# Optimization experiments

Measured on AMD Instinct MI355X. Metric: run time of the kernel, lower is better.

Reference implementation:

```python
import jax, jax.numpy as jnp
import numpy as np

LAMBDA_COORD = 5.0
LAMBDA_NOOBJ = 0.5


def _iou(box1, box2):
    # boxes: [..., 4] in (cx, cy, w, h) format. Matches YoloLoss.IOU:
    # returns 0 when x_right < x_left or y_bottom < y_top (strict),
    # else intersection / (area1 + area2 - intersection).
    x1, y1, w1, h1 = box1[..., 0], box1[..., 1], box1[..., 2], box1[..., 3]
    x2, y2, w2, h2 = box2[..., 0], box2[..., 1], box2[..., 2], box2[..., 3]
    x_left = jnp.maximum(x1 - w1 / 2, x2 - w2 / 2)
    y_top = jnp.maximum(y1 - h1 / 2, y2 - h2 / 2)
    x_right = jnp.minimum(x1 + w1 / 2, x2 + w2 / 2)
    y_bottom = jnp.minimum(y1 + h1 / 2, y2 + h2 / 2)
    valid = jnp.logical_and(x_right >= x_left, y_bottom >= y_top)
    inter = (x_right - x_left) * (y_bottom - y_top)
    union = w1 * h1 + w2 * h2 - inter
    safe_union = jnp.where(union == 0, 1.0, union)
    return jnp.where(valid, inter / safe_union, 0.0)


def setup_inputs() -> dict:
    key = jax.random.key(0)
    k1, k2 = jax.random.split(key)
    B, S, D = 16384, 7, 30  # D = 2*5 + 20
    y = jax.random.normal(k1, (B, S, S, D), dtype=jnp.float32)
    gt = jax.random.normal(k2, (B, S, S, D), dtype=jnp.float32)
    return {"y": y, "gt": gt}


def reference(y, gt):
    pred, target = y, gt
    batch_size = pred.shape[0]
    obj = (target[..., 4] > 0).astype(pred.dtype)      # [B,S,S]
    noobj = (target[..., 4] == 0).astype(pred.dtype)   # [B,S,S]

    # class loss (mask over class channels, indices 10:)
    class_loss = jnp.sum(obj[..., None] * (target[..., 10:] - pred[..., 10:]) ** 2)

    # no-object confidence loss (channel 4, mask before responsibility edits)
    conf_loss_no_obj = jnp.sum(noobj * (target[..., 4] - pred[..., 4]) ** 2)

    # per-cell IOU of target box vs both predicted boxes
    tbox = target[..., 0:4]
    iou1 = _iou(tbox, pred[..., 0:4])   # [B,S,S]
    iou2 = _iou(tbox, pred[..., 5:9])   # [B,S,S]

    # responsibility: keep box1 iff iou1 > iou2 (ties -> box2), as in the torch loop
    resp1 = (iou1 > iou2).astype(pred.dtype)
    m1 = obj * resp1          # box1 responsible mask
    m2 = obj * (1.0 - resp1)  # box2 responsible mask

    # object confidence loss: confidence target is the IOU of the responsible box
    conf_loss_obj = jnp.sum(m1 * (iou1 - pred[..., 4]) ** 2
                            + m2 * (iou2 - pred[..., 9]) ** 2)

    # xy loss (channels 0,1 / 5,6)
    xy_loss = jnp.sum(m1 * ((target[..., 0] - pred[..., 0]) ** 2
                            + (target[..., 1] - pred[..., 1]) ** 2)
                      + m2 * ((target[..., 0] - pred[..., 5]) ** 2
                              + (target[..., 1] - pred[..., 6]) ** 2))

    # wh loss (channels 2,3 / 7,8)
    wh_loss = jnp.sum(m1 * ((target[..., 2] - pred[..., 2]) ** 2
                            + (target[..., 3] - pred[..., 3]) ** 2)
                      + m2 * ((target[..., 2] - pred[..., 7]) ** 2
                              + (target[..., 3] - pred[..., 8]) ** 2))

    total = (LAMBDA_COORD * xy_loss + LAMBDA_COORD * wh_loss
             + conf_loss_obj + LAMBDA_NOOBJ * conf_loss_no_obj
             + class_loss) / batch_size
    return total
```

## Files before the change

### kernel.cpp

```cpp
#include <hip/hip_runtime.h>

#define LAMBDA_COORD 5.0f
#define LAMBDA_NOOBJ 0.5f
#define DD 30
#define BLOCK 64
#define CELLS 64
#define ITERS 4
#define F4C (CELLS * DD / 4)

__device__ __forceinline__ float iou_t(float tx, float ty, float tw, float th,
                                       float px, float py, float pw, float ph) {
    float xl = fmaxf(tx - tw * 0.5f, px - pw * 0.5f);
    float yt = fmaxf(ty - th * 0.5f, py - ph * 0.5f);
    float xr = fminf(tx + tw * 0.5f, px + pw * 0.5f);
    float yb = fminf(ty + th * 0.5f, py + ph * 0.5f);
    bool valid = (xr >= xl) && (yb >= yt);
    float inter = (xr - xl) * (yb - yt);
    float uni = tw * th + pw * ph - inter;
    float safe = (uni == 0.0f) ? 1.0f : uni;
    return valid ? (inter / safe) : 0.0f;
}

__global__ __launch_bounds__(BLOCK) void yolo_loss_kernel(
    const float* __restrict__ pred, const float* __restrict__ targ,
    float* __restrict__ out) {
    __shared__ __align__(16) float sp[CELLS * DD];
    __shared__ __align__(16) float st[CELLS * DD];

    const int tid = threadIdx.x;
    const float4* gp = (const float4*)pred + (size_t)blockIdx.x * (ITERS * F4C);
    const float4* gt = (const float4*)targ + (size_t)blockIdx.x * (ITERS * F4C);
    float4* lp = (float4*)sp;
    float4* lt = (float4*)st;

    float4 rp[8], rt[8];
#pragma unroll
    for (int j = 0; j < 7; ++j) { rp[j] = gp[j * 64 + tid]; rt[j] = gt[j * 64 + tid]; }
    if (tid < 32) { rp[7] = gp[448 + tid]; rt[7] = gt[448 + tid]; }

    float acc = 0.0f;

#pragma unroll
    for (int it = 0; it < ITERS; ++it) {
        asm volatile("" ::: "memory");
#pragma unroll
        for (int j = 0; j < 7; ++j) { lp[j * 64 + tid] = rp[j]; lt[j * 64 + tid] = rt[j]; }
        if (tid < 32) { lp[448 + tid] = rp[7]; lt[448 + tid] = rt[7]; }
        asm volatile("" ::: "memory");

        if (it + 1 < ITERS) {
            const float4* ngp = gp + (size_t)(it + 1) * F4C;
            const float4* ngt = gt + (size_t)(it + 1) * F4C;
#pragma unroll
            for (int j = 0; j < 7; ++j) { rp[j] = ngp[j * 64 + tid]; rt[j] = ngt[j * 64 + tid]; }
            if (tid < 32) { rp[7] = ngp[448 + tid]; rt[7] = ngt[448 + tid]; }
        }
        asm volatile("" ::: "memory");

        const float* p = &sp[tid * DD];
        const float* t = &st[tid * DD];

        float t4 = t[4];
        float obj = (t4 > 0.0f) ? 1.0f : 0.0f;
        float noobj = (t4 == 0.0f) ? 1.0f : 0.0f;

        float cls = 0.0f;
#pragma unroll
        for (int k = 10; k < 30; ++k) {
            float d = t[k] - p[k];
            cls += d * d;
        }
        cls *= obj;

        float d4 = t4 - p[4];
        float conf_noobj = noobj * d4 * d4;

        float tx = t[0], ty = t[1], tw = t[2], th = t[3];
        float iou1 = iou_t(tx, ty, tw, th, p[0], p[1], p[2], p[3]);
        float iou2 = iou_t(tx, ty, tw, th, p[5], p[6], p[7], p[8]);
        float resp1 = (iou1 > iou2) ? 1.0f : 0.0f;
        float m1 = obj * resp1;
        float m2 = obj * (1.0f - resp1);

        float e1 = iou1 - p[4];
        float e2 = iou2 - p[9];
        float conf_obj = m1 * e1 * e1 + m2 * e2 * e2;

        float dx1 = tx - p[0], dy1 = ty - p[1];
        float dx2 = tx - p[5], dy2 = ty - p[6];
        float xy = m1 * (dx1 * dx1 + dy1 * dy1) + m2 * (dx2 * dx2 + dy2 * dy2);

        float dw1 = tw - p[2], dh1 = th - p[3];
        float dw2 = tw - p[7], dh2 = th - p[8];
        float wh = m1 * (dw1 * dw1 + dh1 * dh1) + m2 * (dw2 * dw2 + dh2 * dh2);

        acc += LAMBDA_COORD * (xy + wh) + conf_obj + LAMBDA_NOOBJ * conf_noobj + cls;
    }

#pragma unroll
    for (int off = 32; off > 0; off >>= 1) acc += __shfl_down(acc, off);
    if (tid == 0) atomicAdd(out, acc * (1.0f / 16384.0f));
}

extern "C" void kernel_launch(void* const* d_in, const int* in_sizes, int n_in,
                              void* d_out, int out_size, void* d_ws, size_t ws_size,
                              hipStream_t stream) {
    const float* pred = (const float*)d_in[0];
    const float* targ = (const float*)d_in[1];
    float* out = (float*)d_out;

    hipMemsetAsync(out, 0, sizeof(float), stream);

    const int cells = in_sizes[0] / DD;
    const int grid = cells / (CELLS * ITERS);
    yolo_loss_kernel<<<grid, BLOCK, 0, stream>>>(pred, targ, out);
}
```

Baseline: 236.4 us.

## Shrink per-block tile to 16 cells and quadruple grid size

Each block now handles 16 cells per iteration instead of 64. Loading is still spread across all 64 threads, but only 16 threads compute loss values. The grid becomes four times larger, with fewer registers per thread and less LDS per block, and launch bounds request higher occupancy. The aim is more blocks in flight to hide memory latency. In exchange, 48 of 64 threads sit idle during compute and there are four times more atomics.

```diff
diff --git a/kernel.cpp b/kernel.cpp
--- a/kernel.cpp
+++ b/kernel.cpp
@@ -4,9 +4,9 @@
 #define LAMBDA_NOOBJ 0.5f
 #define DD 30
 #define BLOCK 64
-#define CELLS 64
+#define CPC 16
 #define ITERS 4
-#define F4C (CELLS * DD / 4)
+#define F4C (CPC * DD / 4)
 
 __device__ __forceinline__ float iou_t(float tx, float ty, float tw, float th,
                                        float px, float py, float pw, float ph) {
@@ -21,80 +21,80 @@
     return valid ? (inter / safe) : 0.0f;
 }
 
-__global__ __launch_bounds__(BLOCK) void yolo_loss_kernel(
+__global__ __launch_bounds__(BLOCK, 6) void yolo_loss_kernel(
     const float* __restrict__ pred, const float* __restrict__ targ,
     float* __restrict__ out) {
-    __shared__ __align__(16) float sp[CELLS * DD];
-    __shared__ __align__(16) float st[CELLS * DD];
+    __shared__ __align__(16) float sp[CPC * DD];
+    __shared__ __align__(16) float st[CPC * DD];
 
     const int tid = threadIdx.x;
-    const float4* gp = (const float4*)pred + (size_t)blockIdx.x * (ITERS * F4C);
-    const float4* gt = (const float4*)targ + (size_t)blockIdx.x * (ITERS * F4C);
+    const float4* gp0 = (const float4*)pred + (size_t)blockIdx.x * (ITERS * F4C);
+    const float4* gt0 = (const float4*)targ + (size_t)blockIdx.x * (ITERS * F4C);
     float4* lp = (float4*)sp;
     float4* lt = (float4*)st;
 
-    float4 rp[8], rt[8];
-#pragma unroll
-    for (int j = 0; j < 7; ++j) { rp[j] = gp[j * 64 + tid]; rt[j] = gt[j * 64 + tid]; }
-    if (tid < 32) { rp[7] = gp[448 + tid]; rt[7] = gt[448 + tid]; }
+    const bool act1 = tid < (F4C - 64);
+
+    float4 RP0, RP1, RT0, RT1;
+    RP0 = gp0[tid]; RT0 = gt0[tid];
+    if (act1) { RP1 = gp0[64 + tid]; RT1 = gt0[64 + tid]; }
 
     float acc = 0.0f;
 
 #pragma unroll
     for (int it = 0; it < ITERS; ++it) {
-        asm volatile("" ::: "memory");
-#pragma unroll
-        for (int j = 0; j < 7; ++j) { lp[j * 64 + tid] = rp[j]; lt[j * 64 + tid] = rt[j]; }
-        if (tid < 32) { lp[448 + tid] = rp[7]; lt[448 + tid] = rt[7]; }
-        asm volatile("" ::: "memory");
+        lp[tid] = RP0; lt[tid] = RT0;
+        if (act1) { lp[64 + tid] = RP1; lt[64 + tid] = RT1; }
 
         if (it + 1 < ITERS) {
-            const float4* ngp = gp + (size_t)(it + 1) * F4C;
-            const float4* ngt = gt + (size_t)(it + 1) * F4C;
+            const float4* gp = gp0 + (size_t)(it + 1) * F4C;
+            const float4* gt = gt0 + (size_t)(it + 1) * F4C;
+            RP0 = gp[tid]; RT0 = gt[tid];
+            if (act1) { RP1 = gp[64 + tid]; RT1 = gt[64 + tid]; }
+        }
+
+        float v = 0.0f;
+        if (tid < CPC) {
+            const float* p = &sp[tid * DD];
+            const float* t = &st[tid * DD];
+
+            float t4 = t[4];
+            float obj = (t4 > 0.0f) ? 1.0f : 0.0f;
+            float noobj = (t4 == 0.0f) ? 1.0f : 0.0f;
+
+            float cls = 0.0f;
 #pragma unroll
-            for (int j = 0; j < 7; ++j) { rp[j] = ngp[j * 64 + tid]; rt[j] = ngt[j * 64 + tid]; }
-            if (tid < 32) { rp[7] = ngp[448 + tid]; rt[7] = ngt[448 + tid]; }
+            for (int k = 10; k < 30; ++k) {
+                float d = t[k] - p[k];
+                cls += d * d;
+            }
+            cls *= obj;
+
+            float d4 = t4 - p[4];
+            float conf_noobj = noobj * d4 * d4;
+
+            float tx = t[0], ty = t[1], tw = t[2], th = t[3];
+            float iou1 = iou_t(tx, ty, tw, th, p[0], p[1], p[2], p[3]);
+            float iou2 = iou_t(tx, ty, tw, th, p[5], p[6], p[7], p[8]);
+            float resp1 = (iou1 > iou2) ? 1.0f : 0.0f;
+            float m1 = obj * resp1;
+            float m2 = obj * (1.0f - resp1);
+
+            float e1 = iou1 - p[4];
+            float e2 = iou2 - p[9];
+            float conf_obj = m1 * e1 * e1 + m2 * e2 * e2;
+
+            float dx1 = tx - p[0], dy1 = ty - p[1];
+            float dx2 = tx - p[5], dy2 = ty - p[6];
+            float xy = m1 * (dx1 * dx1 + dy1 * dy1) + m2 * (dx2 * dx2 + dy2 * dy2);
+
+            float dw1 = tw - p[2], dh1 = th - p[3];
+            float dw2 = tw - p[7], dh2 = th - p[8];
+            float wh = m1 * (dw1 * dw1 + dh1 * dh1) + m2 * (dw2 * dw2 + dh2 * dh2);
+
+            v = LAMBDA_COORD * (xy + wh) + conf_obj + LAMBDA_NOOBJ * conf_noobj + cls;
         }
-        asm volatile("" ::: "memory");
-
-        const float* p = &sp[tid * DD];
-        const float* t = &st[tid * DD];
-
-        float t4 = t[4];
-        float obj = (t4 > 0.0f) ? 1.0f : 0.0f;
-        float noobj = (t4 == 0.0f) ? 1.0f : 0.0f;
-
-        float cls = 0.0f;
-#pragma unroll
-        for (int k = 10; k < 30; ++k) {
-            float d = t[k] - p[k];
-            cls += d * d;
-        }
-        cls *= obj;
-
-        float d4 = t4 - p[4];
-        float conf_noobj = noobj * d4 * d4;
-
-        float tx = t[0], ty = t[1], tw = t[2], th = t[3];
-        float iou1 = iou_t(tx, ty, tw, th, p[0], p[1], p[2], p[3]);
-        float iou2 = iou_t(tx, ty, tw, th, p[5], p[6], p[7], p[8]);
-        float resp1 = (iou1 > iou2) ? 1.0f : 0.0f;
-        float m1 = obj * resp1;
-        float m2 = obj * (1.0f - resp1);
-
-        float e1 = iou1 - p[4];
-        float e2 = iou2 - p[9];
-        float conf_obj = m1 * e1 * e1 + m2 * e2 * e2;
-
-        float dx1 = tx - p[0], dy1 = ty - p[1];
-        float dx2 = tx - p[5], dy2 = ty - p[6];
-        float xy = m1 * (dx1 * dx1 + dy1 * dy1) + m2 * (dx2 * dx2 + dy2 * dy2);
-
-        float dw1 = tw - p[2], dh1 = th - p[3];
-        float dw2 = tw - p[7], dh2 = th - p[8];
-        float wh = m1 * (dw1 * dw1 + dh1 * dh1) + m2 * (dw2 * dw2 + dh2 * dh2);
-
-        acc += LAMBDA_COORD * (xy + wh) + conf_obj + LAMBDA_NOOBJ * conf_noobj + cls;
+        acc += v;
     }
 
 #pragma unroll
@@ -112,6 +112,6 @@
     hipMemsetAsync(out, 0, sizeof(float), stream);
 
     const int cells = in_sizes[0] / DD;
-    const int grid = cells / (CELLS * ITERS);
+    const int grid = cells / (CPC * ITERS);
     yolo_loss_kernel<<<grid, BLOCK, 0, stream>>>(pred, targ, out);
 }
```

Result: slower. 349.6 us (+47.9%).
